# Performance work log

Hardware: AMD Instinct MI355X
Metric: run time of the kernel (lower is better)

Reference implementation:

```python
import jax, jax.numpy as jnp
import numpy as np

NUM_EMBEDDINGS = 512
EMBEDDING_DIM = 64
COMMITMENT_COST = 0.25


def setup_inputs() -> dict:
    key = jax.random.key(0)
    k1, k2 = jax.random.split(key)
    x = jax.random.normal(k1, (64, 64, 32, 32), dtype=jnp.float32)  # NCHW, C == embedding_dim
    lim = 1.0 / NUM_EMBEDDINGS
    emb = jax.random.uniform(k2, (NUM_EMBEDDINGS, EMBEDDING_DIM), dtype=jnp.float32,
                             minval=-lim, maxval=lim)
    return {"x": x, "emb": emb}


def reference(x, emb):
    # NCHW -> NHWC
    xp = jnp.transpose(x, (0, 2, 3, 1))  # [B,H,W,D]
    B, H, W, D = xp.shape
    flat = xp.reshape(-1, D)  # [N,D]
    dists = (jnp.sum(flat * flat, axis=1, keepdims=True)
             + jnp.sum(emb * emb, axis=1)
             - 2.0 * jnp.matmul(flat, emb.T))
    idx = jnp.argmin(dists, axis=1)  # [N]
    quantized = emb[idx].reshape(B, H, W, D)
    # losses (note: names follow the original module)
    q_latent_loss = jnp.mean((jax.lax.stop_gradient(quantized) - xp) ** 2)
    e_latent_loss = jnp.mean((quantized - jax.lax.stop_gradient(xp)) ** 2)
    loss = e_latent_loss + COMMITMENT_COST * q_latent_loss
    # straight-through estimator
    quantized = xp + jax.lax.stop_gradient(quantized - xp)
    quantized = jnp.transpose(quantized, (0, 3, 1, 2))  # back to NCHW
    return quantized, loss, idx[:, None]
```

## Files before the change

### kernel.cpp

```cpp
#include <hip/hip_runtime.h>
#include <float.h>

#pragma clang fp contract(off)

#define K_EMB   512
#define D_EMB   64
#define Q_ELEMS 4194304
#define NBLK    1024
#define W_SCR   0.5f
#define XROW    65
#define LCAP    1024

typedef _Float16 f16x8 __attribute__((ext_vector_type(8)));
typedef _Float16 f16x2 __attribute__((ext_vector_type(2)));
typedef float    f32x4 __attribute__((ext_vector_type(4)));

__device__ __forceinline__ float np_sumsq64(const float* v) {
    float r[8];
    #pragma unroll
    for (int j = 0; j < 8; ++j) r[j] = v[j] * v[j];
    #pragma unroll
    for (int i = 8; i < 64; i += 8) {
        #pragma unroll
        for (int j = 0; j < 8; ++j) {
            float s = v[i + j] * v[i + j];
            r[j] = r[j] + s;
        }
    }
    return ((r[0] + r[1]) + (r[2] + r[3])) + ((r[4] + r[5]) + (r[6] + r[7]));
}

__global__ __launch_bounds__(256) void vq_prep(const float* __restrict__ emb,
                                               float* __restrict__ t2,
                                               float* __restrict__ t2s512,
                                               f16x8* __restrict__ embA) {
    const int g = blockIdx.x * 256 + threadIdx.x;
    if (g < K_EMB) {
        const float* ep = emb + (g << 6);
        float s = np_sumsq64(ep);
        t2[g]     = s;
        t2s512[g] = 512.0f * s;
    }
    if (g < 4096) {
        const int t = g >> 7;
        const int s = (g >> 6) & 1;
        const int l = g & 63;
        const int code  = t * 16 + (l & 15);
        const int dbase = s * 32 + ((l >> 4) << 3);
        const float* ep = emb + (code << 6) + dbase;
        f16x8 a;
        #pragma unroll
        for (int i = 0; i < 8; ++i) a[i] = (_Float16)(512.0f * ep[i]);
        embA[g] = a;
    }
}

__global__ __launch_bounds__(512) void vq_main(const float* __restrict__ x,
                                               const float* __restrict__ emb,
                                               const float* __restrict__ t2,
                                               const float* __restrict__ t2s512,
                                               const f16x8* __restrict__ embA,
                                               float* __restrict__ out_q,
                                               float* __restrict__ out_idx,
                                               float* __restrict__ partial) {
    const int tid  = threadIdx.x;
    const int lane = tid & 63;
    const int wave = tid >> 6;
    const int pt   = wave & 3;
    const int ch   = wave >> 2;

    __shared__ float xf[64 * XROW];
    __shared__ float t1s[64];
    __shared__ float mwv[8][16];
    __shared__ unsigned long long keys[64];
    __shared__ int   list[LCAP];
    __shared__ int   lcnt;
    __shared__ float red[8];

    {
        const int p = tid & 63;
        const int np_ = blockIdx.x * 64 + p;
        const float* __restrict__ xs = x + (np_ >> 10) * 65536 + (np_ & 1023);
        #pragma unroll
        for (int j = 0; j < 8; ++j) {
            const int d = wave * 8 + j;
            xf[p * XROW + d] = xs[d * 1024];
        }
        if (tid < 64) keys[tid] = 0xFFFFFFFFFFFFFFFFull;
        if (tid == 0) lcnt = 0;
    }
    __syncthreads();

    if (wave == 0) t1s[lane] = np_sumsq64(&xf[lane * XROW]);

    const int bp = 16 * pt + (lane & 15);
    const int bg = lane >> 4;
    f16x8 b0, b1;
    #pragma unroll
    for (int i = 0; i < 8; ++i) {
        b0[i] = (_Float16)xf[bp * XROW + 0 * 32 + bg * 8 + i];
        b1[i] = (_Float16)xf[bp * XROW + 1 * 32 + bg * 8 + i];
    }

    const f32x4 czero = {0.f, 0.f, 0.f, 0.f};
    const float4* __restrict__ t2s4 = (const float4*)t2s512;
    const int t0 = ch * 16;

    f16x2 hv[32];
    float m = FLT_MAX;
    #pragma unroll
    for (int tt = 0; tt < 16; ++tt) {
        const int t = t0 + tt;
        f16x8 a0 = embA[(t * 2 + 0) * 64 + lane];
        f16x8 a1 = embA[(t * 2 + 1) * 64 + lane];
        f32x4 c = __builtin_amdgcn_mfma_f32_16x16x32_f16(a0, b0, czero, 0, 0, 0);
        c = __builtin_amdgcn_mfma_f32_16x16x32_f16(a1, b1, c, 0, 0, 0);
        float4 tv = t2s4[t * 4 + bg];
        float s0 = fmaf(-2.f, c[0], tv.x);
        float s1 = fmaf(-2.f, c[1], tv.y);
        float s2 = fmaf(-2.f, c[2], tv.z);
        float s3 = fmaf(-2.f, c[3], tv.w);
        f16x2 p01, p23;
        p01[0] = (_Float16)s0; p01[1] = (_Float16)s1;
        p23[0] = (_Float16)s2; p23[1] = (_Float16)s3;
        hv[tt * 2 + 0] = p01;
        hv[tt * 2 + 1] = p23;
        m = fminf(m, fminf(fminf(s0, s1), fminf(s2, s3)));
    }
    m = fminf(m, __shfl_xor(m, 16));
    m = fminf(m, __shfl_xor(m, 32));
    if (lane < 16) mwv[wave][lane] = m;
    __syncthreads();

    const float thr = fminf(mwv[pt][lane & 15], mwv[pt + 4][lane & 15]) + W_SCR;

    #pragma unroll
    for (int tt = 0; tt < 16; ++tt) {
        f16x2 p01 = hv[tt * 2 + 0];
        f16x2 p23 = hv[tt * 2 + 1];
        float s0 = (float)p01[0];
        float s1 = (float)p01[1];
        float s2 = (float)p23[0];
        float s3 = (float)p23[1];
        const int kb = (t0 + tt) * 16 + bg * 4;
        if (s0 < thr) { int s = atomicAdd(&lcnt, 1); if (s < LCAP) list[s] = bp * 512 + kb + 0; }
        if (s1 < thr) { int s = atomicAdd(&lcnt, 1); if (s < LCAP) list[s] = bp * 512 + kb + 1; }
        if (s2 < thr) { int s = atomicAdd(&lcnt, 1); if (s < LCAP) list[s] = bp * 512 + kb + 2; }
        if (s3 < thr) { int s = atomicAdd(&lcnt, 1); if (s < LCAP) list[s] = bp * 512 + kb + 3; }
    }
    __syncthreads();

    const int ncand = min(lcnt, LCAP);
    for (int i = tid; i < ncand; i += 512) {
        const int v = list[i];
        const int p = v >> 9;
        const int k = v & 511;
        const float* xp = &xf[p * XROW];
        const float* __restrict__ ep = emb + (k << 6);
        float a = 0.f;
        #pragma unroll
        for (int d = 0; d < D_EMB; ++d) a = fmaf(xp[d], ep[d], a);
        float X = t1s[p] + t2[k];
        float dnp = fmaf(-2.f, a, X);
        unsigned long long key =
            ((unsigned long long)__float_as_uint(dnp) << 32) | (unsigned)k;
        atomicMin(&keys[p], key);
    }
    __syncthreads();

    float acc = 0.f;
    {
        const int p = tid & 63;
        const int n2 = blockIdx.x * 64 + p;
        const int kw = (int)(unsigned)(keys[p] & 0xFFFFFFFFull);
        float* __restrict__ qp = out_q + (n2 >> 10) * 65536 + (n2 & 1023);
        const float4* __restrict__ eq = (const float4*)(emb + (kw << 6) + wave * 8);
        #pragma unroll
        for (int j4 = 0; j4 < 2; ++j4) {
            float4 qv = eq[j4];
            const int d = wave * 8 + j4 * 4;
            float f0 = qv.x - xf[p * XROW + d + 0];
            float f1 = qv.y - xf[p * XROW + d + 1];
            float f2 = qv.z - xf[p * XROW + d + 2];
            float f3 = qv.w - xf[p * XROW + d + 3];
            acc = fmaf(f0, f0, acc);
            acc = fmaf(f1, f1, acc);
            acc = fmaf(f2, f2, acc);
            acc = fmaf(f3, f3, acc);
            qp[(d + 0) * 1024] = qv.x;
            qp[(d + 1) * 1024] = qv.y;
            qp[(d + 2) * 1024] = qv.z;
            qp[(d + 3) * 1024] = qv.w;
        }
        if (wave == 0) out_idx[n2] = (float)kw;
    }

    #pragma unroll
    for (int off = 32; off > 0; off >>= 1) acc += __shfl_down(acc, off);
    if (lane == 0) red[wave] = acc;
    __syncthreads();
    if (tid == 0)
        partial[blockIdx.x] = ((red[0] + red[1]) + (red[2] + red[3]))
                            + ((red[4] + red[5]) + (red[6] + red[7]));
}

__global__ __launch_bounds__(256) void vq_loss(const float* __restrict__ partial,
                                               float* __restrict__ loss) {
    const int t = threadIdx.x;
    float v = (partial[t] + partial[t + 256]) + (partial[t + 512] + partial[t + 768]);
    #pragma unroll
    for (int off = 32; off > 0; off >>= 1) v += __shfl_down(v, off);
    __shared__ float red[4];
    if ((t & 63) == 0) red[t >> 6] = v;
    __syncthreads();
    if (t == 0)
        loss[0] = 1.25f * ((red[0] + red[1]) + (red[2] + red[3])) / (float)Q_ELEMS;
}

extern "C" void kernel_launch(void* const* d_in, const int* in_sizes, int n_in,
                              void* d_out, int out_size, void* d_ws, size_t ws_size,
                              hipStream_t stream) {
    const float* x   = (const float*)d_in[0];
    const float* emb = (const float*)d_in[1];

    float* out_q    = (float*)d_out;
    float* out_loss = (float*)d_out + Q_ELEMS;
    float* out_idx  = (float*)d_out + Q_ELEMS + 1;

    float* t2      = (float*)d_ws;
    float* t2s512  = t2 + K_EMB;
    float* partial = t2s512 + K_EMB;
    f16x8* embA    = (f16x8*)(partial + 1024);

    vq_prep<<<16, 256, 0, stream>>>(emb, t2, t2s512, embA);
    vq_main<<<NBLK, 512, 0, stream>>>(x, emb, t2, t2s512, embA,
                                      out_q, out_idx, partial);
    vq_loss<<<1, 256, 0, stream>>>(partial, out_loss);
}
```

Baseline: 43.48 us.

## Process two tiles per block with x prefetch and fuse final loss reduction

Each block now handles two 64-point tiles, prefetching the next tile's x into registers while computing the current one, and halving the grid to 512 blocks. The separate loss-reduction kernel is removed; the last block to finish, detected via a global atomic counter reset in the prep kernel, sums the partials and writes the loss. This aims to hide global load latency and save one kernel launch, at the cost of larger shared memory use, fewer blocks for parallelism, and an extra barrier per tile.

```diff
diff --git a/kernel.cpp b/kernel.cpp
--- a/kernel.cpp
+++ b/kernel.cpp
@@ -6,7 +6,8 @@
 #define K_EMB   512
 #define D_EMB   64
 #define Q_ELEMS 4194304
-#define NBLK    1024
+#define TPB     2
+#define NBLK    512
 #define W_SCR   0.5f
 #define XROW    65
 #define LCAP    1024
@@ -33,8 +34,10 @@
 __global__ __launch_bounds__(256) void vq_prep(const float* __restrict__ emb,
                                                float* __restrict__ t2,
                                                float* __restrict__ t2s512,
-                                               f16x8* __restrict__ embA) {
+                                               f16x8* __restrict__ embA,
+                                               unsigned int* __restrict__ done) {
     const int g = blockIdx.x * 256 + threadIdx.x;
+    if (g == 0) *done = 0u;
     if (g < K_EMB) {
         const float* ep = emb + (g << 6);
         float s = np_sumsq64(ep);
@@ -62,159 +65,193 @@
                                                const f16x8* __restrict__ embA,
                                                float* __restrict__ out_q,
                                                float* __restrict__ out_idx,
-                                               float* __restrict__ partial) {
+                                               float* __restrict__ partial,
+                                               unsigned int* __restrict__ done,
+                                               float* __restrict__ loss) {
     const int tid  = threadIdx.x;
     const int lane = tid & 63;
     const int wave = tid >> 6;
     const int pt   = wave & 3;
     const int ch   = wave >> 2;
-
-    __shared__ float xf[64 * XROW];
-    __shared__ float t1s[64];
-    __shared__ float mwv[8][16];
-    __shared__ unsigned long long keys[64];
+    const int p    = tid & 63;
+
+    __shared__ float xf[TPB][64 * XROW];
+    __shared__ float t1s[TPB][64];
+    __shared__ float mwv[TPB][8][16];
+    __shared__ unsigned long long keys[TPB][64];
     __shared__ int   list[LCAP];
-    __shared__ int   lcnt;
+    __shared__ int   lcnt[TPB];
     __shared__ float red[8];
+    __shared__ int   lastf;
 
     {
-        const int p = tid & 63;
-        const int np_ = blockIdx.x * 64 + p;
-        const float* __restrict__ xs = x + (np_ >> 10) * 65536 + (np_ & 1023);
-        #pragma unroll
-        for (int j = 0; j < 8; ++j) {
-            const int d = wave * 8 + j;
-            xf[p * XROW + d] = xs[d * 1024];
-        }
-        if (tid < 64) keys[tid] = 0xFFFFFFFFFFFFFFFFull;
-        if (tid == 0) lcnt = 0;
+        const int n0 = (blockIdx.x * TPB) * 64 + p;
+        const float* __restrict__ xs = x + (n0 >> 10) * 65536 + (n0 & 1023);
+        #pragma unroll
+        for (int j = 0; j < 8; ++j)
+            xf[0][p * XROW + wave * 8 + j] = xs[(wave * 8 + j) * 1024];
+        if (tid < 64) keys[0][tid] = 0xFFFFFFFFFFFFFFFFull;
+        if (tid == 0) lcnt[0] = 0;
     }
     __syncthreads();
-
-    if (wave == 0) t1s[lane] = np_sumsq64(&xf[lane * XROW]);
-
-    const int bp = 16 * pt + (lane & 15);
-    const int bg = lane >> 4;
-    f16x8 b0, b1;
-    #pragma unroll
-    for (int i = 0; i < 8; ++i) {
-        b0[i] = (_Float16)xf[bp * XROW + 0 * 32 + bg * 8 + i];
-        b1[i] = (_Float16)xf[bp * XROW + 1 * 32 + bg * 8 + i];
-    }
 
     const f32x4 czero = {0.f, 0.f, 0.f, 0.f};
     const float4* __restrict__ t2s4 = (const float4*)t2s512;
     const int t0 = ch * 16;
-
-    f16x2 hv[32];
-    float m = FLT_MAX;
-    #pragma unroll
-    for (int tt = 0; tt < 16; ++tt) {
-        const int t = t0 + tt;
-        f16x8 a0 = embA[(t * 2 + 0) * 64 + lane];
-        f16x8 a1 = embA[(t * 2 + 1) * 64 + lane];
-        f32x4 c = __builtin_amdgcn_mfma_f32_16x16x32_f16(a0, b0, czero, 0, 0, 0);
-        c = __builtin_amdgcn_mfma_f32_16x16x32_f16(a1, b1, c, 0, 0, 0);
-        float4 tv = t2s4[t * 4 + bg];
-        float s0 = fmaf(-2.f, c[0], tv.x);
-        float s1 = fmaf(-2.f, c[1], tv.y);
-        float s2 = fmaf(-2.f, c[2], tv.z);
-        float s3 = fmaf(-2.f, c[3], tv.w);
-        f16x2 p01, p23;
-        p01[0] = (_Float16)s0; p01[1] = (_Float16)s1;
-        p23[0] = (_Float16)s2; p23[1] = (_Float16)s3;
-        hv[tt * 2 + 0] = p01;
-        hv[tt * 2 + 1] = p23;
-        m = fminf(m, fminf(fminf(s0, s1), fminf(s2, s3)));
-    }
-    m = fminf(m, __shfl_xor(m, 16));
-    m = fminf(m, __shfl_xor(m, 32));
-    if (lane < 16) mwv[wave][lane] = m;
+    const int bp = 16 * pt + (lane & 15);
+    const int bg = lane >> 4;
+
+    float accLoss = 0.f;
+
+    #pragma unroll
+    for (int it = 0; it < TPB; ++it) {
+        const int ti = blockIdx.x * TPB + it;
+
+        float rv[8];
+        if (it + 1 < TPB) {
+            const int n1 = (ti + 1) * 64 + p;
+            const float* __restrict__ xs1 = x + (n1 >> 10) * 65536 + (n1 & 1023);
+            #pragma unroll
+            for (int j = 0; j < 8; ++j) rv[j] = xs1[(wave * 8 + j) * 1024];
+        }
+
+        if (wave == 0) t1s[it][lane] = np_sumsq64(&xf[it][lane * XROW]);
+
+        f16x8 b0, b1;
+        #pragma unroll
+        for (int i = 0; i < 8; ++i) {
+            b0[i] = (_Float16)xf[it][bp * XROW + 0 * 32 + bg * 8 + i];
+            b1[i] = (_Float16)xf[it][bp * XROW + 1 * 32 + bg * 8 + i];
+        }
+
+        f16x2 hv[32];
+        float m = FLT_MAX;
+        #pragma unroll
+        for (int tt = 0; tt < 16; ++tt) {
+            const int t = t0 + tt;
+            f16x8 a0 = embA[(t * 2 + 0) * 64 + lane];
+            f16x8 a1 = embA[(t * 2 + 1) * 64 + lane];
+            f32x4 c = __builtin_amdgcn_mfma_f32_16x16x32_f16(a0, b0, czero, 0, 0, 0);
+            c = __builtin_amdgcn_mfma_f32_16x16x32_f16(a1, b1, c, 0, 0, 0);
+            float4 tv = t2s4[t * 4 + bg];
+            float s0 = fmaf(-2.f, c[0], tv.x);
+            float s1 = fmaf(-2.f, c[1], tv.y);
+            float s2 = fmaf(-2.f, c[2], tv.z);
+            float s3 = fmaf(-2.f, c[3], tv.w);
+            f16x2 p01, p23;
+            p01[0] = (_Float16)s0; p01[1] = (_Float16)s1;
+            p23[0] = (_Float16)s2; p23[1] = (_Float16)s3;
+            hv[tt * 2 + 0] = p01;
+            hv[tt * 2 + 1] = p23;
+            m = fminf(m, fminf(fminf(s0, s1), fminf(s2, s3)));
+        }
+        m = fminf(m, __shfl_xor(m, 16));
+        m = fminf(m, __shfl_xor(m, 32));
+        if (lane < 16) mwv[it][wave][lane] = m;
+        __syncthreads();
+
+        const float thr = fminf(mwv[it][pt][lane & 15],
+                                mwv[it][pt + 4][lane & 15]) + W_SCR;
+
+        #pragma unroll
+        for (int tt = 0; tt < 16; ++tt) {
+            f16x2 p01 = hv[tt * 2 + 0];
+            f16x2 p23 = hv[tt * 2 + 1];
+            float s0 = (float)p01[0];
+            float s1 = (float)p01[1];
+            float s2 = (float)p23[0];
+            float s3 = (float)p23[1];
+            const int kb = (t0 + tt) * 16 + bg * 4;
+            if (s0 < thr) { int s = atomicAdd(&lcnt[it], 1); if (s < LCAP) list[s] = bp * 512 + kb + 0; }
+            if (s1 < thr) { int s = atomicAdd(&lcnt[it], 1); if (s < LCAP) list[s] = bp * 512 + kb + 1; }
+            if (s2 < thr) { int s = atomicAdd(&lcnt[it], 1); if (s < LCAP) list[s] = bp * 512 + kb + 2; }
+            if (s3 < thr) { int s = atomicAdd(&lcnt[it], 1); if (s < LCAP) list[s] = bp * 512 + kb + 3; }
+        }
+        __syncthreads();
+
+        const int ncand = min(lcnt[it], LCAP);
+        for (int i = tid; i < ncand; i += 512) {
+            const int v  = list[i];
+            const int pp = v >> 9;
+            const int k  = v & 511;
+            const float* xp = &xf[it][pp * XROW];
+            const float* __restrict__ ep = emb + (k << 6);
+            float a = 0.f;
+            #pragma unroll
+            for (int d = 0; d < D_EMB; ++d) a = fmaf(xp[d], ep[d], a);
+            float X = t1s[it][pp] + t2[k];
+            float dnp = fmaf(-2.f, a, X);
+            unsigned long long key =
+                ((unsigned long long)__float_as_uint(dnp) << 32) | (unsigned)k;
+            atomicMin(&keys[it][pp], key);
+        }
+        __syncthreads();
+
+        {
+            const int n2 = ti * 64 + p;
+            const int kw = (int)(unsigned)(keys[it][p] & 0xFFFFFFFFull);
+            float* __restrict__ qp = out_q + (n2 >> 10) * 65536 + (n2 & 1023);
+            const float4* __restrict__ eq =
+                (const float4*)(emb + (kw << 6) + wave * 8);
+            #pragma unroll
+            for (int j4 = 0; j4 < 2; ++j4) {
+                float4 qv = eq[j4];
+                const int d = wave * 8 + j4 * 4;
+                float f0 = qv.x - xf[it][p * XROW + d + 0];
+                float f1 = qv.y - xf[it][p * XROW + d + 1];
+                float f2 = qv.z - xf[it][p * XROW + d + 2];
+                float f3 = qv.w - xf[it][p * XROW + d + 3];
+                accLoss = fmaf(f0, f0, accLoss);
+                accLoss = fmaf(f1, f1, accLoss);
+                accLoss = fmaf(f2, f2, accLoss);
+                accLoss = fmaf(f3, f3, accLoss);
+                qp[(d + 0) * 1024] = qv.x;
+                qp[(d + 1) * 1024] = qv.y;
+                qp[(d + 2) * 1024] = qv.z;
+                qp[(d + 3) * 1024] = qv.w;
+            }
+            if (wave == 0) out_idx[n2] = (float)kw;
+        }
+        if (it + 1 < TPB) {
+            #pragma unroll
+            for (int j = 0; j < 8; ++j)
+                xf[it + 1][p * XROW + wave * 8 + j] = rv[j];
+            if (tid < 64) keys[it + 1][tid] = 0xFFFFFFFFFFFFFFFFull;
+            if (tid == 0) lcnt[it + 1] = 0;
+            __syncthreads();
+        }
+    }
+
+    #pragma unroll
+    for (int off = 32; off > 0; off >>= 1) accLoss += __shfl_down(accLoss, off);
+    if (lane == 0) red[wave] = accLoss;
     __syncthreads();
-
-    const float thr = fminf(mwv[pt][lane & 15], mwv[pt + 4][lane & 15]) + W_SCR;
-
-    #pragma unroll
-    for (int tt = 0; tt < 16; ++tt) {
-        f16x2 p01 = hv[tt * 2 + 0];
-        f16x2 p23 = hv[tt * 2 + 1];
-        float s0 = (float)p01[0];
-        float s1 = (float)p01[1];
-        float s2 = (float)p23[0];
-        float s3 = (float)p23[1];
-        const int kb = (t0 + tt) * 16 + bg * 4;
-        if (s0 < thr) { int s = atomicAdd(&lcnt, 1); if (s < LCAP) list[s] = bp * 512 + kb + 0; }
-        if (s1 < thr) { int s = atomicAdd(&lcnt, 1); if (s < LCAP) list[s] = bp * 512 + kb + 1; }
-        if (s2 < thr) { int s = atomicAdd(&lcnt, 1); if (s < LCAP) list[s] = bp * 512 + kb + 2; }
-        if (s3 < thr) { int s = atomicAdd(&lcnt, 1); if (s < LCAP) list[s] = bp * 512 + kb + 3; }
-    }
-    __syncthreads();
-
-    const int ncand = min(lcnt, LCAP);
-    for (int i = tid; i < ncand; i += 512) {
-        const int v = list[i];
-        const int p = v >> 9;
-        const int k = v & 511;
-        const float* xp = &xf[p * XROW];
-        const float* __restrict__ ep = emb + (k << 6);
-        float a = 0.f;
-        #pragma unroll
-        for (int d = 0; d < D_EMB; ++d) a = fmaf(xp[d], ep[d], a);
-        float X = t1s[p] + t2[k];
-        float dnp = fmaf(-2.f, a, X);
-        unsigned long long key =
-            ((unsigned long long)__float_as_uint(dnp) << 32) | (unsigned)k;
-        atomicMin(&keys[p], key);
-    }
-    __syncthreads();
-
-    float acc = 0.f;
-    {
-        const int p = tid & 63;
-        const int n2 = blockIdx.x * 64 + p;
-        const int kw = (int)(unsigned)(keys[p] & 0xFFFFFFFFull);
-        float* __restrict__ qp = out_q + (n2 >> 10) * 65536 + (n2 & 1023);
-        const float4* __restrict__ eq = (const float4*)(emb + (kw << 6) + wave * 8);
-        #pragma unroll
-        for (int j4 = 0; j4 < 2; ++j4) {
-            float4 qv = eq[j4];
-            const int d = wave * 8 + j4 * 4;
-            float f0 = qv.x - xf[p * XROW + d + 0];
-            float f1 = qv.y - xf[p * XROW + d + 1];
-            float f2 = qv.z - xf[p * XROW + d + 2];
-            float f3 = qv.w - xf[p * XROW + d + 3];
-            acc = fmaf(f0, f0, acc);
-            acc = fmaf(f1, f1, acc);
-            acc = fmaf(f2, f2, acc);
-            acc = fmaf(f3, f3, acc);
-            qp[(d + 0) * 1024] = qv.x;
-            qp[(d + 1) * 1024] = qv.y;
-            qp[(d + 2) * 1024] = qv.z;
-            qp[(d + 3) * 1024] = qv.w;
-        }
-        if (wave == 0) out_idx[n2] = (float)kw;
-    }
-
-    #pragma unroll
-    for (int off = 32; off > 0; off >>= 1) acc += __shfl_down(acc, off);
-    if (lane == 0) red[wave] = acc;
-    __syncthreads();
-    if (tid == 0)
+    if (tid == 0) {
         partial[blockIdx.x] = ((red[0] + red[1]) + (red[2] + red[3]))
                             + ((red[4] + red[5]) + (red[6] + red[7]));
-}
-
-__global__ __launch_bounds__(256) void vq_loss(const float* __restrict__ partial,
-                                               float* __restrict__ loss) {
-    const int t = threadIdx.x;
-    float v = (partial[t] + partial[t + 256]) + (partial[t + 512] + partial[t + 768]);
-    #pragma unroll
-    for (int off = 32; off > 0; off >>= 1) v += __shfl_down(v, off);
-    __shared__ float red[4];
-    if ((t & 63) == 0) red[t >> 6] = v;
+        __threadfence();
+        unsigned int old = atomicAdd(done, 1u);
+        lastf = (old == NBLK - 1) ? 1 : 0;
+    }
     __syncthreads();
-    if (t == 0)
-        loss[0] = 1.25f * ((red[0] + red[1]) + (red[2] + red[3])) / (float)Q_ELEMS;
+
+    if (lastf) {
+        __threadfence();
+        float v = 0.f;
+        if (tid < 256) {
+            float a = __hip_atomic_load(&partial[tid], __ATOMIC_RELAXED,
+                                        __HIP_MEMORY_SCOPE_AGENT);
+            float b = __hip_atomic_load(&partial[tid + 256], __ATOMIC_RELAXED,
+                                        __HIP_MEMORY_SCOPE_AGENT);
+            v = a + b;
+        }
+        #pragma unroll
+        for (int off = 32; off > 0; off >>= 1) v += __shfl_down(v, off);
+        if (lane == 0 && wave < 4) red[wave] = v;
+        __syncthreads();
+        if (tid == 0)
+            loss[0] = 1.25f * ((red[0] + red[1]) + (red[2] + red[3])) / (float)Q_ELEMS;
+    }
 }
 
 extern "C" void kernel_launch(void* const* d_in, const int* in_sizes, int n_in,
@@ -227,13 +264,13 @@
     float* out_loss = (float*)d_out + Q_ELEMS;
     float* out_idx  = (float*)d_out + Q_ELEMS + 1;
 
-    float* t2      = (float*)d_ws;
-    float* t2s512  = t2 + K_EMB;
-    float* partial = t2s512 + K_EMB;
-    f16x8* embA    = (f16x8*)(partial + 1024);
-
-    vq_prep<<<16, 256, 0, stream>>>(emb, t2, t2s512, embA);
+    float*        t2      = (float*)d_ws;
+    float*        t2s512  = t2 + K_EMB;
+    float*        partial = t2s512 + K_EMB;
+    unsigned int* done    = (unsigned int*)(partial + 512);
+    f16x8*        embA    = (f16x8*)((float*)d_ws + 2048);
+
+    vq_prep<<<16, 256, 0, stream>>>(emb, t2, t2s512, embA, done);
     vq_main<<<NBLK, 512, 0, stream>>>(x, emb, t2, t2s512, embA,
-                                      out_q, out_idx, partial);
-    vq_loss<<<1, 256, 0, stream>>>(partial, out_loss);
-}
+                                      out_q, out_idx, partial, done, out_loss);
+}
```

After: 66.30 us. 1.52x slower.

## Fuse loss reduction into main kernel and double point tiles per wave

Applied to the files above, without the earlier changes.

The separate single-block loss kernel is removed. Its reduction now runs in whichever main-kernel block finishes last, found through a global atomic counter that the prep kernel resets. Each wave also now computes MFMA tiles for two 16-point groups against half as many codebook tiles, so every loaded embedding A fragment is reused twice. This saves one kernel launch and halves embedding fragment loads per wave, at the cost of more registers for the doubled score arrays and a serial tail in the last block.

```diff
diff --git a/kernel.cpp b/kernel.cpp
--- a/kernel.cpp
+++ b/kernel.cpp
@@ -33,8 +33,10 @@
 __global__ __launch_bounds__(256) void vq_prep(const float* __restrict__ emb,
                                                float* __restrict__ t2,
                                                float* __restrict__ t2s512,
-                                               f16x8* __restrict__ embA) {
+                                               f16x8* __restrict__ embA,
+                                               unsigned int* __restrict__ done) {
     const int g = blockIdx.x * 256 + threadIdx.x;
+    if (g == 0) *done = 0u;
     if (g < K_EMB) {
         const float* ep = emb + (g << 6);
         float s = np_sumsq64(ep);
@@ -62,30 +64,31 @@
                                                const f16x8* __restrict__ embA,
                                                float* __restrict__ out_q,
                                                float* __restrict__ out_idx,
-                                               float* __restrict__ partial) {
+                                               float* __restrict__ partial,
+                                               unsigned int* __restrict__ done,
+                                               float* __restrict__ loss) {
     const int tid  = threadIdx.x;
     const int lane = tid & 63;
     const int wave = tid >> 6;
-    const int pt   = wave & 3;
-    const int ch   = wave >> 2;
+    const int pg   = wave & 1;
+    const int cq   = wave >> 1;
+    const int p    = tid & 63;
 
     __shared__ float xf[64 * XROW];
     __shared__ float t1s[64];
-    __shared__ float mwv[8][16];
+    __shared__ float mwv[8][2][16];
     __shared__ unsigned long long keys[64];
     __shared__ int   list[LCAP];
     __shared__ int   lcnt;
     __shared__ float red[8];
+    __shared__ int   lastf;
 
     {
-        const int p = tid & 63;
         const int np_ = blockIdx.x * 64 + p;
         const float* __restrict__ xs = x + (np_ >> 10) * 65536 + (np_ & 1023);
         #pragma unroll
-        for (int j = 0; j < 8; ++j) {
-            const int d = wave * 8 + j;
-            xf[p * XROW + d] = xs[d * 1024];
-        }
+        for (int j = 0; j < 8; ++j)
+            xf[p * XROW + wave * 8 + j] = xs[(wave * 8 + j) * 1024];
         if (tid < 64) keys[tid] = 0xFFFFFFFFFFFFFFFFull;
         if (tid == 0) lcnt = 0;
     }
@@ -93,84 +96,108 @@
 
     if (wave == 0) t1s[lane] = np_sumsq64(&xf[lane * XROW]);
 
-    const int bp = 16 * pt + (lane & 15);
-    const int bg = lane >> 4;
-    f16x8 b0, b1;
+    const int bp0 = 32 * pg + (lane & 15);
+    const int bp1 = bp0 + 16;
+    const int bg  = lane >> 4;
+    f16x8 b00, b01, b10, b11;
     #pragma unroll
     for (int i = 0; i < 8; ++i) {
-        b0[i] = (_Float16)xf[bp * XROW + 0 * 32 + bg * 8 + i];
-        b1[i] = (_Float16)xf[bp * XROW + 1 * 32 + bg * 8 + i];
+        b00[i] = (_Float16)xf[bp0 * XROW + 0 * 32 + bg * 8 + i];
+        b01[i] = (_Float16)xf[bp0 * XROW + 1 * 32 + bg * 8 + i];
+        b10[i] = (_Float16)xf[bp1 * XROW + 0 * 32 + bg * 8 + i];
+        b11[i] = (_Float16)xf[bp1 * XROW + 1 * 32 + bg * 8 + i];
     }
 
     const f32x4 czero = {0.f, 0.f, 0.f, 0.f};
     const float4* __restrict__ t2s4 = (const float4*)t2s512;
-    const int t0 = ch * 16;
-
-    f16x2 hv[32];
-    float m = FLT_MAX;
-    #pragma unroll
-    for (int tt = 0; tt < 16; ++tt) {
+    const int t0 = cq * 8;
+
+    f16x2 hv0[16], hv1[16];
+    float m0 = FLT_MAX, m1 = FLT_MAX;
+    #pragma unroll
+    for (int tt = 0; tt < 8; ++tt) {
         const int t = t0 + tt;
         f16x8 a0 = embA[(t * 2 + 0) * 64 + lane];
         f16x8 a1 = embA[(t * 2 + 1) * 64 + lane];
-        f32x4 c = __builtin_amdgcn_mfma_f32_16x16x32_f16(a0, b0, czero, 0, 0, 0);
-        c = __builtin_amdgcn_mfma_f32_16x16x32_f16(a1, b1, c, 0, 0, 0);
+        f32x4 c0 = __builtin_amdgcn_mfma_f32_16x16x32_f16(a0, b00, czero, 0, 0, 0);
+        c0 = __builtin_amdgcn_mfma_f32_16x16x32_f16(a1, b01, c0, 0, 0, 0);
+        f32x4 c1 = __builtin_amdgcn_mfma_f32_16x16x32_f16(a0, b10, czero, 0, 0, 0);
+        c1 = __builtin_amdgcn_mfma_f32_16x16x32_f16(a1, b11, c1, 0, 0, 0);
         float4 tv = t2s4[t * 4 + bg];
-        float s0 = fmaf(-2.f, c[0], tv.x);
-        float s1 = fmaf(-2.f, c[1], tv.y);
-        float s2 = fmaf(-2.f, c[2], tv.z);
-        float s3 = fmaf(-2.f, c[3], tv.w);
-        f16x2 p01, p23;
-        p01[0] = (_Float16)s0; p01[1] = (_Float16)s1;
-        p23[0] = (_Float16)s2; p23[1] = (_Float16)s3;
-        hv[tt * 2 + 0] = p01;
-        hv[tt * 2 + 1] = p23;
-        m = fminf(m, fminf(fminf(s0, s1), fminf(s2, s3)));
-    }
-    m = fminf(m, __shfl_xor(m, 16));
-    m = fminf(m, __shfl_xor(m, 32));
-    if (lane < 16) mwv[wave][lane] = m;
-    __syncthreads();
-
-    const float thr = fminf(mwv[pt][lane & 15], mwv[pt + 4][lane & 15]) + W_SCR;
-
-    #pragma unroll
-    for (int tt = 0; tt < 16; ++tt) {
-        f16x2 p01 = hv[tt * 2 + 0];
-        f16x2 p23 = hv[tt * 2 + 1];
-        float s0 = (float)p01[0];
-        float s1 = (float)p01[1];
-        float s2 = (float)p23[0];
-        float s3 = (float)p23[1];
+        float s00 = fmaf(-2.f, c0[0], tv.x);
+        float s01 = fmaf(-2.f, c0[1], tv.y);
+        float s02 = fmaf(-2.f, c0[2], tv.z);
+        float s03 = fmaf(-2.f, c0[3], tv.w);
+        float s10 = fmaf(-2.f, c1[0], tv.x);
+        float s11 = fmaf(-2.f, c1[1], tv.y);
+        float s12 = fmaf(-2.f, c1[2], tv.z);
+        float s13 = fmaf(-2.f, c1[3], tv.w);
+        f16x2 q0, q1, q2, q3;
+        q0[0] = (_Float16)s00; q0[1] = (_Float16)s01;
+        q1[0] = (_Float16)s02; q1[1] = (_Float16)s03;
+        q2[0] = (_Float16)s10; q2[1] = (_Float16)s11;
+        q3[0] = (_Float16)s12; q3[1] = (_Float16)s13;
+        hv0[tt * 2 + 0] = q0;  hv0[tt * 2 + 1] = q1;
+        hv1[tt * 2 + 0] = q2;  hv1[tt * 2 + 1] = q3;
+        m0 = fminf(m0, fminf(fminf(s00, s01), fminf(s02, s03)));
+        m1 = fminf(m1, fminf(fminf(s10, s11), fminf(s12, s13)));
+    }
+    m0 = fminf(m0, __shfl_xor(m0, 16));
+    m0 = fminf(m0, __shfl_xor(m0, 32));
+    m1 = fminf(m1, __shfl_xor(m1, 16));
+    m1 = fminf(m1, __shfl_xor(m1, 32));
+    if (lane < 16) {
+        mwv[wave][0][lane] = m0;
+        mwv[wave][1][lane] = m1;
+    }
+    __syncthreads();
+
+    const int li = lane & 15;
+    const float thr0 = fminf(fminf(mwv[pg][0][li],     mwv[pg + 2][0][li]),
+                             fminf(mwv[pg + 4][0][li], mwv[pg + 6][0][li])) + W_SCR;
+    const float thr1 = fminf(fminf(mwv[pg][1][li],     mwv[pg + 2][1][li]),
+                             fminf(mwv[pg + 4][1][li], mwv[pg + 6][1][li])) + W_SCR;
+
+    #pragma unroll
+    for (int tt = 0; tt < 8; ++tt) {
         const int kb = (t0 + tt) * 16 + bg * 4;
-        if (s0 < thr) { int s = atomicAdd(&lcnt, 1); if (s < LCAP) list[s] = bp * 512 + kb + 0; }
-        if (s1 < thr) { int s = atomicAdd(&lcnt, 1); if (s < LCAP) list[s] = bp * 512 + kb + 1; }
-        if (s2 < thr) { int s = atomicAdd(&lcnt, 1); if (s < LCAP) list[s] = bp * 512 + kb + 2; }
-        if (s3 < thr) { int s = atomicAdd(&lcnt, 1); if (s < LCAP) list[s] = bp * 512 + kb + 3; }
+        f16x2 q0 = hv0[tt * 2 + 0], q1 = hv0[tt * 2 + 1];
+        f16x2 q2 = hv1[tt * 2 + 0], q3 = hv1[tt * 2 + 1];
+        float s00 = (float)q0[0], s01 = (float)q0[1];
+        float s02 = (float)q1[0], s03 = (float)q1[1];
+        float s10 = (float)q2[0], s11 = (float)q2[1];
+        float s12 = (float)q3[0], s13 = (float)q3[1];
+        if (s00 < thr0) { int s = atomicAdd(&lcnt, 1); if (s < LCAP) list[s] = bp0 * 512 + kb + 0; }
+        if (s01 < thr0) { int s = atomicAdd(&lcnt, 1); if (s < LCAP) list[s] = bp0 * 512 + kb + 1; }
+        if (s02 < thr0) { int s = atomicAdd(&lcnt, 1); if (s < LCAP) list[s] = bp0 * 512 + kb + 2; }
+        if (s03 < thr0) { int s = atomicAdd(&lcnt, 1); if (s < LCAP) list[s] = bp0 * 512 + kb + 3; }
+        if (s10 < thr1) { int s = atomicAdd(&lcnt, 1); if (s < LCAP) list[s] = bp1 * 512 + kb + 0; }
+        if (s11 < thr1) { int s = atomicAdd(&lcnt, 1); if (s < LCAP) list[s] = bp1 * 512 + kb + 1; }
+        if (s12 < thr1) { int s = atomicAdd(&lcnt, 1); if (s < LCAP) list[s] = bp1 * 512 + kb + 2; }
+        if (s13 < thr1) { int s = atomicAdd(&lcnt, 1); if (s < LCAP) list[s] = bp1 * 512 + kb + 3; }
     }
     __syncthreads();
 
     const int ncand = min(lcnt, LCAP);
     for (int i = tid; i < ncand; i += 512) {
-        const int v = list[i];
-        const int p = v >> 9;
-        const int k = v & 511;
-        const float* xp = &xf[p * XROW];
+        const int v  = list[i];
+        const int pp = v >> 9;
+        const int k  = v & 511;
+        const float* xp = &xf[pp * XROW];
         const float* __restrict__ ep = emb + (k << 6);
         float a = 0.f;
         #pragma unroll
         for (int d = 0; d < D_EMB; ++d) a = fmaf(xp[d], ep[d], a);
-        float X = t1s[p] + t2[k];
+        float X = t1s[pp] + t2[k];
         float dnp = fmaf(-2.f, a, X);
         unsigned long long key =
             ((unsigned long long)__float_as_uint(dnp) << 32) | (unsigned)k;
-        atomicMin(&keys[p], key);
+        atomicMin(&keys[pp], key);
     }
     __syncthreads();
 
     float acc = 0.f;
     {
-        const int p = tid & 63;
         const int n2 = blockIdx.x * 64 + p;
         const int kw = (int)(unsigned)(keys[p] & 0xFFFFFFFFull);
         float* __restrict__ qp = out_q + (n2 >> 10) * 65536 + (n2 & 1023);
@@ -199,22 +226,30 @@
     for (int off = 32; off > 0; off >>= 1) acc += __shfl_down(acc, off);
     if (lane == 0) red[wave] = acc;
     __syncthreads();
-    if (tid == 0)
+    if (tid == 0) {
         partial[blockIdx.x] = ((red[0] + red[1]) + (red[2] + red[3]))
                             + ((red[4] + red[5]) + (red[6] + red[7]));
-}
-
-__global__ __launch_bounds__(256) void vq_loss(const float* __restrict__ partial,
-                                               float* __restrict__ loss) {
-    const int t = threadIdx.x;
-    float v = (partial[t] + partial[t + 256]) + (partial[t + 512] + partial[t + 768]);
-    #pragma unroll
-    for (int off = 32; off > 0; off >>= 1) v += __shfl_down(v, off);
-    __shared__ float red[4];
-    if ((t & 63) == 0) red[t >> 6] = v;
-    __syncthreads();
-    if (t == 0)
-        loss[0] = 1.25f * ((red[0] + red[1]) + (red[2] + red[3])) / (float)Q_ELEMS;
+        __threadfence();
+        unsigned int old = atomicAdd(done, 1u);
+        lastf = (old == NBLK - 1) ? 1 : 0;
+    }
+    __syncthreads();
+
+    if (lastf) {
+        __threadfence();
+        float a = __hip_atomic_load(&partial[tid], __ATOMIC_RELAXED,
+                                    __HIP_MEMORY_SCOPE_AGENT);
+        float b = __hip_atomic_load(&partial[tid + 512], __ATOMIC_RELAXED,
+                                    __HIP_MEMORY_SCOPE_AGENT);
+        float v = a + b;
+        #pragma unroll
+        for (int off = 32; off > 0; off >>= 1) v += __shfl_down(v, off);
+        if (lane == 0) red[wave] = v;
+        __syncthreads();
+        if (tid == 0)
+            loss[0] = 1.25f * (((red[0] + red[1]) + (red[2] + red[3]))
+                             + ((red[4] + red[5]) + (red[6] + red[7]))) / (float)Q_ELEMS;
+    }
 }
 
 extern "C" void kernel_launch(void* const* d_in, const int* in_sizes, int n_in,
@@ -227,13 +262,13 @@
     float* out_loss = (float*)d_out + Q_ELEMS;
     float* out_idx  = (float*)d_out + Q_ELEMS + 1;
 
-    float* t2      = (float*)d_ws;
-    float* t2s512  = t2 + K_EMB;
-    float* partial = t2s512 + K_EMB;
-    f16x8* embA    = (f16x8*)(partial + 1024);
-
-    vq_prep<<<16, 256, 0, stream>>>(emb, t2, t2s512, embA);
+    float*        t2      = (float*)d_ws;
+    float*        t2s512  = t2 + K_EMB;
+    float*        partial = t2s512 + K_EMB;
+    unsigned int* done    = (unsigned int*)(partial + 1024);
+    f16x8*        embA    = (f16x8*)((float*)d_ws + 2560);
+
+    vq_prep<<<16, 256, 0, stream>>>(emb, t2, t2s512, embA, done);
     vq_main<<<NBLK, 512, 0, stream>>>(x, emb, t2, t2s512, embA,
-                                      out_q, out_idx, partial);
-    vq_loss<<<1, 256, 0, stream>>>(partial, out_loss);
-}
+                                      out_q, out_idx, partial, done, out_loss);
+}
```

Result: slower. 76.21 us (+75.3%).
